# Kernel optimization log

Measured on AMD Instinct MI355X. Metric: run time of the kernel, lower is better.

The kernel has to match this reference:

```python
import jax, jax.numpy as jnp
import numpy as np

EPS = 1e-5

def layer_norm(x, gamma, beta):
    mu = jnp.mean(x, axis=-1, keepdims=True)
    var = jnp.mean(jnp.square(x - mu), axis=-1, keepdims=True)
    return (x - mu) * jax.lax.rsqrt(var + EPS) * gamma + beta

def setup_inputs() -> dict:
    key = jax.random.key(0)
    ks = jax.random.split(key, 12)
    B, S, D = 2, 4096, 1024
    H = 4 * D
    s_in = 1.0 / np.sqrt(D)
    s_h = 1.0 / np.sqrt(H)
    return {
        "input_embedding": jax.random.normal(ks[0], (B, S, D), dtype=jnp.float32),
        "Wq": jax.random.uniform(ks[1], (D, D), jnp.float32, -s_in, s_in),
        "bq": jax.random.uniform(ks[2], (D,), jnp.float32, -s_in, s_in),
        "Wk": jax.random.uniform(ks[3], (D, D), jnp.float32, -s_in, s_in),
        "bk": jax.random.uniform(ks[4], (D,), jnp.float32, -s_in, s_in),
        "Wv": jax.random.uniform(ks[5], (D, D), jnp.float32, -s_in, s_in),
        "bv": jax.random.uniform(ks[6], (D,), jnp.float32, -s_in, s_in),
        "W1": jax.random.uniform(ks[7], (D, H), jnp.float32, -s_in, s_in),
        "b1": jax.random.uniform(ks[8], (H,), jnp.float32, -s_in, s_in),
        "W2": jax.random.uniform(ks[9], (H, D), jnp.float32, -s_h, s_h),
        "b2": jax.random.uniform(ks[10], (D,), jnp.float32, -s_h, s_h),
        "gamma": jnp.ones((D,), jnp.float32),
        "beta": jnp.zeros((D,), jnp.float32),
    }

def reference(input_embedding, Wq, bq, Wk, bk, Wv, bv, W1, b1, W2, b2, gamma, beta):
    D = input_embedding.shape[-1]
    # projections
    k = input_embedding @ Wk + bk
    q = input_embedding @ Wq + bq
    v = input_embedding @ Wv + bv
    # NOTE: original calls attention(k, q, v) so Q<-k, K<-q, V<-v (faithful quirk)
    scores = jnp.einsum('bsd,btd->bst', k, q) / jnp.sqrt(jnp.float32(D))
    attn = jax.nn.softmax(scores, axis=-1)
    attn_out = jnp.einsum('bst,btd->bsd', attn, v)  # dropout = identity (eval)
    x = layer_norm(input_embedding + attn_out, gamma, beta)
    # feed-forward (GELU exact, dropout identity)
    h = jax.nn.gelu(x @ W1 + b1, approximate=False)
    ff = h @ W2 + b2
    return layer_norm(x + ff, gamma, beta)
```

## Files before the change

kernel.cpp:

```cpp
#include <hip/hip_runtime.h>
#include <hip/hip_bf16.h>
#include <stdint.h>

#define AS1 __attribute__((address_space(1)))
#define AS3 __attribute__((address_space(3)))

typedef __bf16 bf16x8 __attribute__((ext_vector_type(8)));
typedef __bf16 bf16x4 __attribute__((ext_vector_type(4)));
typedef float  f32x4  __attribute__((ext_vector_type(4)));

__device__ __forceinline__ void gld_lds16(const void* g, void* l) {
    __builtin_amdgcn_global_load_lds((AS1 void*)g, (AS3 void*)l, 16, 0, 0);
}

__device__ __forceinline__ void xcd_remap(int& bc, int& br) {
    const int GX = gridDim.x, GY = gridDim.y;
    const int L = blockIdx.y * GX + blockIdx.x;
    int rw, rh, nregx;
    if (GX >= 16 && (GX & 1) == 0 && (GY & 3) == 0) {
        rw = GX >> 1; rh = GY >> 2; nregx = 2;
    } else if ((GY & 7) == 0) {
        rw = GX;      rh = GY >> 3; nregx = 1;
    } else {
        bc = blockIdx.x; br = blockIdx.y; return;
    }
    const int xcd  = L & 7;
    const int slot = L >> 3;
    const int rx = xcd % nregx, ry = xcd / nregx;
    bc = rx * rw + slot % rw;
    br = ry * rh + slot / rw;
}

__global__ __launch_bounds__(256, 4)
void gemm_nt(const __bf16* __restrict__ A, const __bf16* __restrict__ B,
             __bf16* __restrict__ C, const float* __restrict__ bias,
             float* __restrict__ rowsum,
             int K, int lda, int ldb, int ldc,
             long sA, long sB, long sC, long sBias,
             int ep, float scale)
{
    __shared__ __bf16 smA[2][4096];
    __shared__ __bf16 smB[2][4096];
    const int t  = threadIdx.x;
    const int l  = t & 63;
    const int w  = t >> 6;
    const int wm = w >> 1, wn = w & 1;
    const int lr = l & 15;
    const int lq = l >> 4;
    const long bz = blockIdx.z;
    int br, bc;
    xcd_remap(bc, br);

    const int swc = ((t & 3) ^ ((t >> 3) & 3)) * 8;
    const __bf16* ag = A + bz * sA + (size_t)(br * 128 + (t >> 2)) * lda + swc;
    const __bf16* bg = B + bz * sB + (size_t)(bc * 128 + (t >> 2)) * ldb + swc;
    const size_t a64 = (size_t)64 * lda, b64 = (size_t)64 * ldb;

    f32x4 acc[4][4];
    const f32x4 zero4 = {0.f, 0.f, 0.f, 0.f};
#pragma unroll
    for (int i = 0; i < 4; ++i)
#pragma unroll
        for (int j = 0; j < 4; ++j) acc[i][j] = zero4;

    const int paOff = (wm * 64 + lr) * 32 + ((lq ^ ((lr >> 1) & 3)) * 8);
    const int pbOff = (wn * 64 + lr) * 32 + ((lq ^ ((lr >> 1) & 3)) * 8);

    auto prefetch = [&](int b) {
        __bf16* la = &smA[b][t * 8];
        __bf16* lb = &smB[b][t * 8];
        gld_lds16(ag,       la);
        gld_lds16(ag + a64, la + 2048);
        gld_lds16(bg,       lb);
        gld_lds16(bg + b64, lb + 2048);
        ag += 32; bg += 32;
    };
    auto compute = [&](int b) {
        const __bf16* pa = &smA[b][paOff];
        const __bf16* pb = &smB[b][pbOff];
        bf16x8 af[4], bfr[4];
#pragma unroll
        for (int i = 0; i < 4; ++i) af[i]  = *(const bf16x8*)(pa + i * 16 * 32);
#pragma unroll
        for (int j = 0; j < 4; ++j) bfr[j] = *(const bf16x8*)(pb + j * 16 * 32);
#pragma unroll
        for (int i = 0; i < 4; ++i)
#pragma unroll
            for (int j = 0; j < 4; ++j)
                acc[i][j] = __builtin_amdgcn_mfma_f32_16x16x32_bf16(af[i], bfr[j], acc[i][j], 0, 0, 0);
    };

    const int nkt = K >> 5;
    prefetch(0);
    for (int kt = 0; kt < nkt; kt += 2) {
        __syncthreads();
        if (kt + 1 < nkt) prefetch(1);
        compute(0);
        __syncthreads();
        if (kt + 2 < nkt) prefetch(0);
        compute(1);
    }

    const int r0 = br * 128 + wm * 64 + lq * 4;
    const int c0 = bc * 128 + wn * 64 + lr;
    C += bz * sC;

    if (ep == 4) {
#pragma unroll
        for (int i = 0; i < 4; ++i) {
            float rs4[4] = {0.f, 0.f, 0.f, 0.f};
#pragma unroll
            for (int j = 0; j < 4; ++j) {
                const int col = c0 + j * 16;
#pragma unroll
                for (int r = 0; r < 4; ++r) {
                    const long row = r0 + i * 16 + r;
                    const float e = __expf(acc[i][j][r] * scale - 8.0f);
                    C[row * (long)ldc + col] = (__bf16)e;
                    rs4[r] += e;
                }
            }
#pragma unroll
            for (int r = 0; r < 4; ++r) {
                float s = rs4[r];
                s += __shfl_xor(s, 1, 64);
                s += __shfl_xor(s, 2, 64);
                s += __shfl_xor(s, 4, 64);
                s += __shfl_xor(s, 8, 64);
                if (lr == 0) atomicAdd(&rowsum[r0 + i * 16 + r], s);
            }
        }
        return;
    }

    const float* bs = bias ? bias + bz * sBias : nullptr;
#pragma unroll
    for (int i = 0; i < 4; ++i) {
#pragma unroll
        for (int j = 0; j < 4; ++j) {
            const int col = c0 + j * 16;
            const float bcol = (ep != 1 && bs) ? bs[col] : 0.f;
#pragma unroll
            for (int r = 0; r < 4; ++r) {
                const long row = r0 + i * 16 + r;
                const long idx = row * (long)ldc + col;
                const float v = acc[i][j][r];
                if (ep == 0) {
                    C[idx] = (__bf16)(v + bcol);
                } else if (ep == 1) {
                    C[idx] = (__bf16)(v * scale);
                } else {
                    const float u = v + bcol;
                    const float z = 1.59576912f * (u + 0.044715f * u * u * u);
                    C[idx] = (__bf16)(u / (1.f + __expf(-z)));
                }
            }
        }
    }
}

__global__ __launch_bounds__(256)
void conv_bf16(const float* __restrict__ in, __bf16* __restrict__ out)
{
    const long i = (long)blockIdx.x * 256 + threadIdx.x;
    const float4 f = ((const float4*)in)[i];
    bf16x4 o = {(__bf16)f.x, (__bf16)f.y, (__bf16)f.z, (__bf16)f.w};
    ((bf16x4*)out)[i] = o;
}

__global__ void tr_f32_bf16(const float* __restrict__ in, __bf16* __restrict__ out,
                            int K, int N)
{
    __shared__ float tl[32][33];
    const int x = threadIdx.x, y = threadIdx.y;
    const int n0 = blockIdx.x * 32, k0 = blockIdx.y * 32;
#pragma unroll
    for (int i = 0; i < 4; ++i)
        tl[y + 8 * i][x] = in[(size_t)(k0 + y + 8 * i) * N + n0 + x];
    __syncthreads();
#pragma unroll
    for (int i = 0; i < 4; ++i)
        out[(size_t)(n0 + y + 8 * i) * K + k0 + x] = (__bf16)tl[x][y + 8 * i];
}

__global__ void tr_bf16(const __bf16* __restrict__ in, __bf16* __restrict__ out,
                        int R, int C)
{
    in  += (size_t)blockIdx.z * R * C;
    out += (size_t)blockIdx.z * R * C;
    __shared__ __bf16 tl[32][33];
    const int x = threadIdx.x, y = threadIdx.y;
    const int c0 = blockIdx.x * 32, r0 = blockIdx.y * 32;
#pragma unroll
    for (int i = 0; i < 4; ++i)
        tl[y + 8 * i][x] = in[(size_t)(r0 + y + 8 * i) * C + c0 + x];
    __syncthreads();
#pragma unroll
    for (int i = 0; i < 4; ++i)
        out[(size_t)(c0 + y + 8 * i) * R + r0 + x] = tl[x][y + 8 * i];
}

__global__ __launch_bounds__(256)
void ln_residual(const float* __restrict__ af, const __bf16* __restrict__ ab,
                 const __bf16* __restrict__ bb, const __bf16* __restrict__ bb2,
                 const __bf16* __restrict__ bb3, const __bf16* __restrict__ bb4,
                 const float* __restrict__ lnb,
                 const float* __restrict__ rowscale,
                 const float* __restrict__ gamma, const float* __restrict__ beta,
                 float* __restrict__ outf, __bf16* __restrict__ outb)
{
    const long row = blockIdx.x;
    const int t = threadIdx.x;
    float x0, x1, x2, x3;
    if (af) {
        const float4 va = ((const float4*)(af + row * 1024))[t];
        x0 = va.x; x1 = va.y; x2 = va.z; x3 = va.w;
    } else {
        const bf16x4 va = ((const bf16x4*)(ab + row * 1024))[t];
        x0 = (float)va[0]; x1 = (float)va[1]; x2 = (float)va[2]; x3 = (float)va[3];
    }
    float p0, p1, p2, p3;
    {
        const bf16x4 vb = ((const bf16x4*)(bb + row * 1024))[t];
        p0 = (float)vb[0]; p1 = (float)vb[1]; p2 = (float)vb[2]; p3 = (float)vb[3];
    }
    if (bb2) {
        const bf16x4 vb = ((const bf16x4*)(bb2 + row * 1024))[t];
        p0 += (float)vb[0]; p1 += (float)vb[1]; p2 += (float)vb[2]; p3 += (float)vb[3];
    }
    if (bb3) {
        const bf16x4 vb = ((const bf16x4*)(bb3 + row * 1024))[t];
        p0 += (float)vb[0]; p1 += (float)vb[1]; p2 += (float)vb[2]; p3 += (float)vb[3];
    }
    if (bb4) {
        const bf16x4 vb = ((const bf16x4*)(bb4 + row * 1024))[t];
        p0 += (float)vb[0]; p1 += (float)vb[1]; p2 += (float)vb[2]; p3 += (float)vb[3];
    }
    if (rowscale) {
        const float inv = 1.f / rowscale[row];
        p0 *= inv; p1 *= inv; p2 *= inv; p3 *= inv;
    }
    x0 += p0; x1 += p1; x2 += p2; x3 += p3;
    if (lnb) {
        const float4 vb = ((const float4*)lnb)[t];
        x0 += vb.x; x1 += vb.y; x2 += vb.z; x3 += vb.w;
    }
    float s = x0 + x1 + x2 + x3;
    float q = x0 * x0 + x1 * x1 + x2 * x2 + x3 * x3;
#pragma unroll
    for (int o = 32; o; o >>= 1) { s += __shfl_down(s, o, 64); q += __shfl_down(q, o, 64); }
    __shared__ float rs[4], rq[4];
    if ((t & 63) == 0) { rs[t >> 6] = s; rq[t >> 6] = q; }
    __syncthreads();
    s = rs[0] + rs[1] + rs[2] + rs[3];
    q = rq[0] + rq[1] + rq[2] + rq[3];
    const float mu  = s * (1.f / 1024.f);
    const float inv = rsqrtf(q * (1.f / 1024.f) - mu * mu + 1e-5f);
    const float4 g  = ((const float4*)gamma)[t];
    const float4 be = ((const float4*)beta)[t];
    const float y0 = (x0 - mu) * inv * g.x + be.x;
    const float y1 = (x1 - mu) * inv * g.y + be.y;
    const float y2 = (x2 - mu) * inv * g.z + be.z;
    const float y3 = (x3 - mu) * inv * g.w + be.w;
    if (outf) ((float4*)(outf + row * 1024))[t] = make_float4(y0, y1, y2, y3);
    if (outb) {
        bf16x4 o4 = {(__bf16)y0, (__bf16)y1, (__bf16)y2, (__bf16)y3};
        ((bf16x4*)outb)[row * 256 + t] = o4;
    }
}

__global__ __launch_bounds__(256)
void fill_diag(float* __restrict__ out, float v, long n)
{
    const long i = (long)blockIdx.x * 256 + threadIdx.x;
    if (i < n) out[i] = v;
}

extern "C" void kernel_launch(void* const* d_in, const int* in_sizes, int n_in,
                              void* d_out, int out_size, void* d_ws, size_t ws_size,
                              hipStream_t stream)
{
    const float* X  = (const float*)d_in[0];
    const float* Wq = (const float*)d_in[1];
    const float* bq = (const float*)d_in[2];
    const float* Wk = (const float*)d_in[3];
    const float* bk = (const float*)d_in[4];
    const float* Wv = (const float*)d_in[5];
    const float* bv = (const float*)d_in[6];
    const float* W1 = (const float*)d_in[7];
    const float* b1 = (const float*)d_in[8];
    const float* W2 = (const float*)d_in[9];
    const float* b2 = (const float*)d_in[10];
    const float* gamma = (const float*)d_in[11];
    const float* beta  = (const float*)d_in[12];
    float* out = (float*)d_out;

    const int S = 4096, D = 1024, H = 4096;
    const int M = 2 * S;
    const size_t MB = 1ull << 20;

    char* ws = (char*)d_ws;
    __bf16* W1T = (__bf16*)(ws);
    __bf16* W2T = (__bf16*)(ws + 8 * MB);
    __bf16* XB  = (__bf16*)(ws + 16 * MB);
    __bf16* P0  = XB;
    __bf16* QP  = (__bf16*)(ws + 32 * MB);
    __bf16* KP  = (__bf16*)(ws + 48 * MB);
    __bf16* VP  = (__bf16*)(ws + 64 * MB);
    float*  RS  = (float*)(ws + 64 * MB);
    __bf16* VT  = (__bf16*)(ws + 80 * MB);
    __bf16* FF  = VT;
    __bf16* HB  = XB;
    __bf16* SL  = (__bf16*)(ws + 96 * MB);
    __bf16* WQT = (__bf16*)(ws + 96 * MB);
    float*  BIAS= (float*)(ws + 96 * MB + 6 * MB);
    __bf16* XLNB= (__bf16*)(ws + 96 * MB);
    __bf16* FF2 = (__bf16*)(ws + 112 * MB);

    int Rs;
    if (ws_size >= 128 * MB)      Rs = 4096;
    else if (ws_size >= 112 * MB) Rs = 2048;
    else {
        fill_diag<<<dim3((out_size + 255) / 256), dim3(256), 0, stream>>>(
            out, (float)(ws_size >> 20), out_size);
        return;
    }

    const dim3 t256(256);
    const dim3 t32x8(32, 8);

    conv_bf16<<<dim3(M * D / 1024), t256, 0, stream>>>(X, XB);
    tr_f32_bf16<<<dim3(D / 32, D / 32), t32x8, 0, stream>>>(Wq, WQT, D, D);
    tr_f32_bf16<<<dim3(D / 32, D / 32), t32x8, 0, stream>>>(Wk, WQT + (size_t)D * D, D, D);
    tr_f32_bf16<<<dim3(D / 32, D / 32), t32x8, 0, stream>>>(Wv, WQT + (size_t)2 * D * D, D, D);
    tr_f32_bf16<<<dim3(H / 32, D / 32), t32x8, 0, stream>>>(W1, W1T, D, H);
    tr_f32_bf16<<<dim3(D / 32, H / 32), t32x8, 0, stream>>>(W2, W2T, H, D);
    hipMemcpyAsync(BIAS,         bq, D * 4, hipMemcpyDeviceToDevice, stream);
    hipMemcpyAsync(BIAS + D,     bk, D * 4, hipMemcpyDeviceToDevice, stream);
    hipMemcpyAsync(BIAS + 2 * D, bv, D * 4, hipMemcpyDeviceToDevice, stream);

    gemm_nt<<<dim3(D / 128, M / 128, 3), t256, 0, stream>>>(
        XB, WQT, QP, BIAS, nullptr, D, D, D, D,
        0, (long)D * D, (long)M * D, D, 0, 0.f);

    tr_bf16<<<dim3(D / 32, S / 32, 2), t32x8, 0, stream>>>(VP, VT, S, D);

    fill_diag<<<dim3(M / 256), t256, 0, stream>>>(RS, 0.f, M);

    const long sCpv = (long)(QP - P0);
    for (int b = 0; b < 2; ++b) {
        for (int c = 0; c < S / Rs; ++c) {
            const __bf16* Ak = KP + (size_t)(b * S + c * Rs) * D;
            gemm_nt<<<dim3(S / 128, Rs / 128), t256, 0, stream>>>(
                Ak, QP + (size_t)b * S * D, SL, nullptr, RS + (size_t)b * S + c * Rs,
                D, D, D, S, 0, 0, 0, 0, 4, 0.03125f);
            gemm_nt<<<dim3(D / 128, Rs / 128, 2), t256, 0, stream>>>(
                SL, VT + (size_t)b * D * S, P0 + (size_t)(b * S + c * Rs) * D, nullptr, nullptr,
                S / 2, S, S, D, S / 2, S / 2, sCpv, 0, 0, 0.f);
        }
    }

    ln_residual<<<dim3(M), t256, 0, stream>>>(
        X, nullptr, P0, QP, nullptr, nullptr, nullptr, RS, gamma, beta, nullptr, XLNB);

    gemm_nt<<<dim3(H / 128, M / 128), t256, 0, stream>>>(
        XLNB, W1T, HB, b1, nullptr, D, D, D, H, 0, 0, 0, 0, 3, 0.f);

    if (Rs == 4096) {
        gemm_nt<<<dim3(D / 128, M / 128, 2), t256, 0, stream>>>(
            HB, W2T, FF, nullptr, nullptr, H / 2, H, H, D,
            H / 2, H / 2, (long)(FF2 - FF), 0, 1, 1.0f);
        ln_residual<<<dim3(M), t256, 0, stream>>>(
            nullptr, XLNB, FF, FF2, nullptr, nullptr, b2, nullptr, gamma, beta, out, nullptr);
    } else {
        gemm_nt<<<dim3(D / 128, M / 128), t256, 0, stream>>>(
            HB, W2T, FF, b2, nullptr, H, H, H, D, 0, 0, 0, 0, 0, 0.f);
        ln_residual<<<dim3(M), t256, 0, stream>>>(
            nullptr, XLNB, FF, nullptr, nullptr, nullptr, nullptr, nullptr, gamma, beta, out, nullptr);
    }
}
```

Baseline: 621.9 us.

## Fuse V transpose into QKV GEMM epilogue and merge weight transposes

The QKV projection GEMM gains an epilogue mode that writes the V slice directly in transposed (b, d, s) layout into the VT buffer, which removes the separate bf16 transpose kernel. The three Wq/Wk/Wv transpose launches become one launch with a z dimension. Row-sum storage moves into the output buffer, and the second split-K partial of the attention-output GEMM now lands in the VP region, which is free because V is no longer stored row-major. The transposed epilogue stores are strided scalar bf16 writes (4096 elements apart), so the write coalescing of that GEMM slice gets worse.

```diff
diff --git a/kernel.cpp b/kernel.cpp
--- a/kernel.cpp
+++ b/kernel.cpp
@@ -104,6 +104,7 @@
     const int r0 = br * 128 + wm * 64 + lq * 4;
     const int c0 = bc * 128 + wn * 64 + lr;
     C += bz * sC;
+    const float* bs = bias ? bias + bz * sBias : nullptr;
 
     if (ep == 4) {
 #pragma unroll
@@ -133,7 +134,26 @@
         return;
     }
 
-    const float* bs = bias ? bias + bz * sBias : nullptr;
+    if (ep == 5 && bz == 2) {
+        __bf16* VT = (__bf16*)rowsum;
+#pragma unroll
+        for (int i = 0; i < 4; ++i) {
+#pragma unroll
+            for (int j = 0; j < 4; ++j) {
+                const int col = c0 + j * 16;
+                const float bcol = bs ? bs[col] : 0.f;
+#pragma unroll
+                for (int r = 0; r < 4; ++r) {
+                    const long row = r0 + i * 16 + r;
+                    const long b   = row >> 12;
+                    const long s   = row & 4095;
+                    VT[(b * 1024 + col) * 4096 + s] = (__bf16)(acc[i][j][r] + bcol);
+                }
+            }
+        }
+        return;
+    }
+
 #pragma unroll
     for (int i = 0; i < 4; ++i) {
 #pragma unroll
@@ -145,7 +165,7 @@
                 const long row = r0 + i * 16 + r;
                 const long idx = row * (long)ldc + col;
                 const float v = acc[i][j][r];
-                if (ep == 0) {
+                if (ep == 0 || ep == 5) {
                     C[idx] = (__bf16)(v + bcol);
                 } else if (ep == 1) {
                     C[idx] = (__bf16)(v * scale);
@@ -183,21 +203,23 @@
         out[(size_t)(n0 + y + 8 * i) * K + k0 + x] = (__bf16)tl[x][y + 8 * i];
 }
 
-__global__ void tr_bf16(const __bf16* __restrict__ in, __bf16* __restrict__ out,
-                        int R, int C)
-{
-    in  += (size_t)blockIdx.z * R * C;
-    out += (size_t)blockIdx.z * R * C;
-    __shared__ __bf16 tl[32][33];
+__global__ void tr3_f32_bf16(const float* __restrict__ in0,
+                             const float* __restrict__ in1,
+                             const float* __restrict__ in2,
+                             __bf16* __restrict__ out, int D)
+{
+    const float* in = (blockIdx.z == 0) ? in0 : (blockIdx.z == 1) ? in1 : in2;
+    out += (size_t)blockIdx.z * D * D;
+    __shared__ float tl[32][33];
     const int x = threadIdx.x, y = threadIdx.y;
-    const int c0 = blockIdx.x * 32, r0 = blockIdx.y * 32;
+    const int n0 = blockIdx.x * 32, k0 = blockIdx.y * 32;
 #pragma unroll
     for (int i = 0; i < 4; ++i)
-        tl[y + 8 * i][x] = in[(size_t)(r0 + y + 8 * i) * C + c0 + x];
+        tl[y + 8 * i][x] = in[(size_t)(k0 + y + 8 * i) * D + n0 + x];
     __syncthreads();
 #pragma unroll
     for (int i = 0; i < 4; ++i)
-        out[(size_t)(c0 + y + 8 * i) * R + r0 + x] = tl[x][y + 8 * i];
+        out[(size_t)(n0 + y + 8 * i) * D + k0 + x] = (__bf16)tl[x][y + 8 * i];
 }
 
 __global__ __launch_bounds__(256)
@@ -307,7 +329,6 @@
     __bf16* QP  = (__bf16*)(ws + 32 * MB);
     __bf16* KP  = (__bf16*)(ws + 48 * MB);
     __bf16* VP  = (__bf16*)(ws + 64 * MB);
-    float*  RS  = (float*)(ws + 64 * MB);
     __bf16* VT  = (__bf16*)(ws + 80 * MB);
     __bf16* FF  = VT;
     __bf16* HB  = XB;
@@ -316,6 +337,7 @@
     float*  BIAS= (float*)(ws + 96 * MB + 6 * MB);
     __bf16* XLNB= (__bf16*)(ws + 96 * MB);
     __bf16* FF2 = (__bf16*)(ws + 112 * MB);
+    float*  RS  = out;
 
     int Rs;
     if (ws_size >= 128 * MB)      Rs = 4096;
@@ -330,9 +352,7 @@
     const dim3 t32x8(32, 8);
 
     conv_bf16<<<dim3(M * D / 1024), t256, 0, stream>>>(X, XB);
-    tr_f32_bf16<<<dim3(D / 32, D / 32), t32x8, 0, stream>>>(Wq, WQT, D, D);
-    tr_f32_bf16<<<dim3(D / 32, D / 32), t32x8, 0, stream>>>(Wk, WQT + (size_t)D * D, D, D);
-    tr_f32_bf16<<<dim3(D / 32, D / 32), t32x8, 0, stream>>>(Wv, WQT + (size_t)2 * D * D, D, D);
+    tr3_f32_bf16<<<dim3(D / 32, D / 32, 3), t32x8, 0, stream>>>(Wq, Wk, Wv, WQT, D);
     tr_f32_bf16<<<dim3(H / 32, D / 32), t32x8, 0, stream>>>(W1, W1T, D, H);
     tr_f32_bf16<<<dim3(D / 32, H / 32), t32x8, 0, stream>>>(W2, W2T, H, D);
     hipMemcpyAsync(BIAS,         bq, D * 4, hipMemcpyDeviceToDevice, stream);
@@ -340,14 +360,12 @@
     hipMemcpyAsync(BIAS + 2 * D, bv, D * 4, hipMemcpyDeviceToDevice, stream);
 
     gemm_nt<<<dim3(D / 128, M / 128, 3), t256, 0, stream>>>(
-        XB, WQT, QP, BIAS, nullptr, D, D, D, D,
-        0, (long)D * D, (long)M * D, D, 0, 0.f);
-
-    tr_bf16<<<dim3(D / 32, S / 32, 2), t32x8, 0, stream>>>(VP, VT, S, D);
+        XB, WQT, QP, BIAS, (float*)VT, D, D, D, D,
+        0, (long)D * D, (long)M * D, D, 5, 0.f);
 
     fill_diag<<<dim3(M / 256), t256, 0, stream>>>(RS, 0.f, M);
 
-    const long sCpv = (long)(QP - P0);
+    const long sCpv = (long)(VP - P0);
     for (int b = 0; b < 2; ++b) {
         for (int c = 0; c < S / Rs; ++c) {
             const __bf16* Ak = KP + (size_t)(b * S + c * Rs) * D;
@@ -355,13 +373,14 @@
                 Ak, QP + (size_t)b * S * D, SL, nullptr, RS + (size_t)b * S + c * Rs,
                 D, D, D, S, 0, 0, 0, 0, 4, 0.03125f);
             gemm_nt<<<dim3(D / 128, Rs / 128, 2), t256, 0, stream>>>(
-                SL, VT + (size_t)b * D * S, P0 + (size_t)(b * S + c * Rs) * D, nullptr, nullptr,
+                SL, VT + (size_t)b * D * S, P0 + (size_t)(b * S + c * Rs) * D,
+                nullptr, nullptr,
                 S / 2, S, S, D, S / 2, S / 2, sCpv, 0, 0, 0.f);
         }
     }
 
     ln_residual<<<dim3(M), t256, 0, stream>>>(
-        X, nullptr, P0, QP, nullptr, nullptr, nullptr, RS, gamma, beta, nullptr, XLNB);
+        X, nullptr, P0, VP, nullptr, nullptr, nullptr, RS, gamma, beta, nullptr, XLNB);
 
     gemm_nt<<<dim3(H / 128, M / 128), t256, 0, stream>>>(
         XLNB, W1T, HB, b1, nullptr, D, D, D, H, 0, 0, 0, 0, 3, 0.f);
```

Measured after the change: 647.9 us. 1.04x slower.
